# Optimization experiments

Hardware: AMD Instinct MI355X
Metric: run time of the kernel (lower is better)

## Reference

```python
import jax, jax.numpy as jnp
import numpy as np

L = 4          # layers_num
N_HIPER = 30   # n_hiper
S = 4096       # number of ray samples
D = 768        # embedding width (hardcoded in source)


def setup_inputs() -> dict:
    key = jax.random.key(0)
    k1, k2, k3 = jax.random.split(key, 3)
    # coords must lie in [-L, L] so grid indices stay in [0, 2L]
    samples = jax.random.uniform(k1, (S, 2), minval=-float(L), maxval=float(L), dtype=jnp.float32)
    last_point = jax.random.uniform(k2, (2,), minval=-float(L), maxval=float(L), dtype=jnp.float32)
    embeddings = jax.random.normal(k3, (2 * L + 1, 2 * L + 1, N_HIPER + 1, D), dtype=jnp.float32)
    return {"samples": samples, "last_point": last_point, "embeddings": embeddings}


def reference(samples, last_point, embeddings):
    x, y = samples[:, 0], samples[:, 1]
    # fractional parts computed BEFORE the +L shift, exactly as in the source
    dx = (x - jnp.floor(x))[:, None, None]  # [S,1,1]
    dy = (y - jnp.floor(y))[:, None, None]
    xs, ys = x + L, y + L
    fx = jnp.floor(xs).astype(jnp.int32)
    cx = jnp.ceil(xs).astype(jnp.int32)
    fy = jnp.floor(ys).astype(jnp.int32)
    cy = jnp.ceil(ys).astype(jnp.int32)
    # batched bilinear gather: each corner lookup is [S, N_HIPER+1, D]
    above = embeddings[fx, cy] * (1.0 - dx) + embeddings[cx, cy] * dx
    below = embeddings[fx, fy] * (1.0 - dx) + embeddings[cx, fy] * dx
    emb = below * (1.0 - dy) + above * dy  # [S, N_HIPER+1, D]

    # distance to next sample; last sample measures to last_point
    nxt = jnp.concatenate([samples[1:], last_point[None, :]], axis=0)
    dists = jnp.linalg.norm(nxt - samples, axis=1)  # [S]

    density = jax.nn.relu(emb[:, N_HIPER])          # [S, D] (per-channel density)
    dd = density * dists[:, None]                   # [S, D]
    # Ti uses EXCLUSIVE cumsum: summed_density is updated after Ti is read
    cum_excl = jnp.concatenate(
        [jnp.zeros((1, D), dd.dtype), jnp.cumsum(dd, axis=0)[:-1]], axis=0
    )
    weights = jnp.exp(-cum_excl) * (1.0 - jnp.exp(-dd))  # Ti * alpha, [S, D]
    # sum_s weights[s,d] * emb[s,n,d]  -> [N_HIPER, D]
    return jnp.einsum("sd,snd->nd", weights, emb[:, :N_HIPER])
```

## Files before the change

kernel.cpp:

```cpp
#include <hip/hip_runtime.h>
#include <math.h>

#define NS 4096
#define DD 768
#define NH 30
#define NCH 31
#define NCELL 81
#define NBLK 256
#define NTHR 384
#define CS 16
#define NPART 6
#define SPP 683
#define NW (NCELL*DD)
#define NACC (NCELL*NPART)

__global__ __launch_bounds__(NTHR) void pass1_kernel(
    const float* __restrict__ samples, const float* __restrict__ last_point,
    const float* __restrict__ emb,
    int4* __restrict__ cells, float4* __restrict__ coefs,
    float* __restrict__ ddbuf, float* __restrict__ chunk_sum,
    float* __restrict__ W)
{
    __shared__ int4   s_cells[CS];
    __shared__ float4 s_coefs[CS];
    __shared__ float  s_dist[CS];

    const int t  = threadIdx.x;
    const int b  = blockIdx.x;
    const int d0 = 2*t;

    if (t < CS) {
        const int s = b*CS + t;
        float x = samples[2*s+0], y = samples[2*s+1];
        float xs = x + 4.0f, ys = y + 4.0f;
        int fx = (int)floorf(xs), cx = (int)ceilf(xs);
        int fy = (int)floorf(ys), cy = (int)ceilf(ys);
        float dx = x - floorf(x), dy = y - floorf(y);
        float nx, ny;
        if (s == NS-1) { nx = last_point[0]; ny = last_point[1]; }
        else           { nx = samples[2*s+2]; ny = samples[2*s+3]; }
        float ex = nx - x, ey = ny - y;
        s_dist[t] = sqrtf(ex*ex + ey*ey);
        int4 cl = make_int4(fx*9+fy, cx*9+fy, fx*9+cy, cx*9+cy);
        float4 cf = make_float4((1.f-dx)*(1.f-dy), dx*(1.f-dy),
                                (1.f-dx)*dy,       dx*dy);
        s_cells[t] = cl; s_coefs[t] = cf;
        cells[s] = cl;   coefs[s]  = cf;
    }
    { int g = b*NTHR + t; if (g < NW) W[g] = 0.f; }
    __syncthreads();

    float sx = 0.f, sy = 0.f;
    #pragma unroll
    for (int i = 0; i < CS; ++i) {
        int4 cl = s_cells[i]; float4 cf = s_coefs[i]; float dist = s_dist[i];
        const int off = NH*DD + d0;
        float2 e0 = *(const float2*)(emb + cl.x*NCH*DD + off);
        float2 e1 = *(const float2*)(emb + cl.y*NCH*DD + off);
        float2 e2 = *(const float2*)(emb + cl.z*NCH*DD + off);
        float2 e3 = *(const float2*)(emb + cl.w*NCH*DD + off);
        float vx = e0.x*cf.x + e1.x*cf.y + e2.x*cf.z + e3.x*cf.w;
        float vy = e0.y*cf.x + e1.y*cf.y + e2.y*cf.z + e3.y*cf.w;
        float ddx = fmaxf(vx, 0.f) * dist;
        float ddy = fmaxf(vy, 0.f) * dist;
        *(float2*)(ddbuf + (b*CS + i)*DD + d0) = make_float2(ddx, ddy);
        sx += ddx; sy += ddy;
    }
    *(float2*)(chunk_sum + b*DD + d0) = make_float2(sx, sy);
}

__global__ __launch_bounds__(64) void scan_kernel(
    const float* __restrict__ chunk_sum, float* __restrict__ offs) {
    const int d    = blockIdx.x;
    const int lane = threadIdx.x;
    float v[4];
    #pragma unroll
    for (int k = 0; k < 4; ++k)
        v[k] = chunk_sum[(lane*4 + k)*DD + d];
    float tot = (v[0] + v[1]) + (v[2] + v[3]);
    float x = tot;
    #pragma unroll
    for (int off = 1; off < 64; off <<= 1) {
        float y = __shfl_up(x, off);
        if (lane >= off) x += y;
    }
    float run = x - tot;
    #pragma unroll
    for (int k = 0; k < 4; ++k) {
        offs[(lane*4 + k)*DD + d] = run;
        run += v[k];
    }
}

__global__ __launch_bounds__(NTHR) void w_kernel(
    const float* __restrict__ ddbuf, const float* __restrict__ offs,
    float* __restrict__ w) {
    const int t  = threadIdx.x;
    const int b  = blockIdx.x;
    const int d0 = 2*t;
    float2 cum = *(const float2*)(offs + b*DD + d0);
    float Ex = __expf(-cum.x), Ey = __expf(-cum.y);
    #pragma unroll
    for (int i = 0; i < CS; ++i) {
        float2 dd = *(const float2*)(ddbuf + (b*CS + i)*DD + d0);
        float fx = __expf(-dd.x), fy = __expf(-dd.y);
        *(float2*)(w + (b*CS + i)*DD + d0) =
            make_float2(Ex * (1.f - fx), Ey * (1.f - fy));
        Ex *= fx; Ey *= fy;
    }
}

__global__ __launch_bounds__(256) void wacc_kernel(
    const int4* __restrict__ cells, const float4* __restrict__ coefs,
    const float* __restrict__ w, float* __restrict__ W) {
    __shared__ int   s_idx[SPP];
    __shared__ float s_cf[SPP];
    __shared__ int   s_cnt;
    const int g    = blockIdx.x / NPART;
    const int part = blockIdx.x % NPART;
    const int t    = threadIdx.x;
    if (t == 0) s_cnt = 0;
    __syncthreads();
    const int s_beg = part * SPP;
    const int s_end = min(NS, s_beg + SPP);
    for (int s = s_beg + t; s < s_end; s += 256) {
        int4 cl = cells[s]; float4 cf = coefs[s];
        float c = 0.f;
        if (cl.x == g) c += cf.x;
        if (cl.y == g) c += cf.y;
        if (cl.z == g) c += cf.z;
        if (cl.w == g) c += cf.w;
        if (c != 0.f) {
            int idx = atomicAdd(&s_cnt, 1);
            s_idx[idx] = s;
            s_cf[idx]  = c;
        }
    }
    __syncthreads();
    const int cnt = s_cnt;
    float a0 = 0.f, a1 = 0.f, a2 = 0.f;
    for (int j = 0; j < cnt; ++j) {
        const float* wr = w + (long)s_idx[j]*DD;
        const float  c  = s_cf[j];
        a0 += c * wr[t];
        a1 += c * wr[t + 256];
        a2 += c * wr[t + 512];
    }
    atomicAdd(&W[g*DD + t      ], a0);
    atomicAdd(&W[g*DD + t + 256], a1);
    atomicAdd(&W[g*DD + t + 512], a2);
}

__global__ __launch_bounds__(256) void final_kernel(
    const float* __restrict__ emb, const float* __restrict__ W,
    float* __restrict__ out) {
    const int n    = blockIdx.x / 3;
    const int part = blockIdx.x % 3;
    const int d    = part*256 + threadIdx.x;
    float a0 = 0.f, a1 = 0.f, a2 = 0.f, a3 = 0.f;
    int g = 0;
    #pragma unroll 4
    for (; g + 4 <= 80; g += 4) {
        a0 += W[(g+0)*DD + d] * emb[((g+0)*NCH + n)*DD + d];
        a1 += W[(g+1)*DD + d] * emb[((g+1)*NCH + n)*DD + d];
        a2 += W[(g+2)*DD + d] * emb[((g+2)*NCH + n)*DD + d];
        a3 += W[(g+3)*DD + d] * emb[((g+3)*NCH + n)*DD + d];
    }
    a0 += W[80*DD + d] * emb[(80*NCH + n)*DD + d];
    out[n*DD + d] = (a0 + a1) + (a2 + a3);
}

extern "C" void kernel_launch(void* const* d_in, const int* in_sizes, int n_in,
                              void* d_out, int out_size, void* d_ws, size_t ws_size,
                              hipStream_t stream) {
    const float* samples    = (const float*)d_in[0];
    const float* last_point = (const float*)d_in[1];
    const float* emb        = (const float*)d_in[2];
    float* out = (float*)d_out;

    char* ws = (char*)d_ws;
    int4*   cells  = (int4*)ws;     ws += (size_t)NS*sizeof(int4);
    float4* coefs  = (float4*)ws;   ws += (size_t)NS*sizeof(float4);
    float*  chunk_sum = (float*)ws; ws += (size_t)NBLK*DD*sizeof(float);
    float*  offs   = (float*)ws;    ws += (size_t)NBLK*DD*sizeof(float);
    float*  Wbuf   = (float*)ws;    ws += (size_t)NW*sizeof(float);
    float*  ddbuf  = (float*)ws;    ws += (size_t)NS*DD*sizeof(float);
    float*  wmat   = (float*)ws;    ws += (size_t)NS*DD*sizeof(float);

    pass1_kernel<<<NBLK, NTHR, 0, stream>>>(samples, last_point, emb,
                                            cells, coefs, ddbuf, chunk_sum,
                                            Wbuf);
    scan_kernel<<<DD, 64, 0, stream>>>(chunk_sum, offs);
    w_kernel<<<NBLK, NTHR, 0, stream>>>(ddbuf, offs, wmat);
    wacc_kernel<<<NACC, 256, 0, stream>>>(cells, coefs, wmat, Wbuf);
    final_kernel<<<NH*3, 256, 0, stream>>>(emb, Wbuf, out);
}
```

Before: 38.08 us.

## Replace additive density scan with multiplicative transmittance scan and drop w kernel

pass1 now computes per-chunk local transmittance products and unscaled weights directly. The scan runs over products of exp factors instead of sums. The chunk scale is applied inside the accumulation kernel, which removes the separate w_kernel and one full S×D intermediate buffer. Loads are widened to float4 and the final kernel is reorganised to one block per output row. The cost is a product-based scan that can underflow differently from the sum-then-exp form, plus a changed chunk and thread geometry.

Result: slower. 49.57 us (+30.2%).

```diff
diff --git a/kernel.cpp b/kernel.cpp
--- a/kernel.cpp
+++ b/kernel.cpp
@@ -6,9 +6,9 @@
 #define NH 30
 #define NCH 31
 #define NCELL 81
-#define NBLK 256
-#define NTHR 384
-#define CS 16
+#define NBLK 512
+#define NTHR 192
+#define CS 8
 #define NPART 6
 #define SPP 683
 #define NW (NCELL*DD)
@@ -18,7 +18,7 @@
     const float* __restrict__ samples, const float* __restrict__ last_point,
     const float* __restrict__ emb,
     int4* __restrict__ cells, float4* __restrict__ coefs,
-    float* __restrict__ ddbuf, float* __restrict__ chunk_sum,
+    float* __restrict__ u, float* __restrict__ Ebuf,
     float* __restrict__ W)
 {
     __shared__ int4   s_cells[CS];
@@ -27,7 +27,7 @@
 
     const int t  = threadIdx.x;
     const int b  = blockIdx.x;
-    const int d0 = 2*t;
+    const int d0 = 4*t;
 
     if (t < CS) {
         const int s = b*CS + t;
@@ -47,83 +47,78 @@
         s_cells[t] = cl; s_coefs[t] = cf;
         cells[s] = cl;   coefs[s]  = cf;
     }
-    { int g = b*NTHR + t; if (g < NW) W[g] = 0.f; }
+    {
+        int g = b*NTHR + t; if (g < NW) W[g] = 0.f;
+    }
     __syncthreads();
 
-    float sx = 0.f, sy = 0.f;
+    float4 E = make_float4(1.f, 1.f, 1.f, 1.f);
     #pragma unroll
     for (int i = 0; i < CS; ++i) {
         int4 cl = s_cells[i]; float4 cf = s_coefs[i]; float dist = s_dist[i];
         const int off = NH*DD + d0;
-        float2 e0 = *(const float2*)(emb + cl.x*NCH*DD + off);
-        float2 e1 = *(const float2*)(emb + cl.y*NCH*DD + off);
-        float2 e2 = *(const float2*)(emb + cl.z*NCH*DD + off);
-        float2 e3 = *(const float2*)(emb + cl.w*NCH*DD + off);
+        float4 e0 = *(const float4*)(emb + cl.x*NCH*DD + off);
+        float4 e1 = *(const float4*)(emb + cl.y*NCH*DD + off);
+        float4 e2 = *(const float4*)(emb + cl.z*NCH*DD + off);
+        float4 e3 = *(const float4*)(emb + cl.w*NCH*DD + off);
         float vx = e0.x*cf.x + e1.x*cf.y + e2.x*cf.z + e3.x*cf.w;
         float vy = e0.y*cf.x + e1.y*cf.y + e2.y*cf.z + e3.y*cf.w;
-        float ddx = fmaxf(vx, 0.f) * dist;
-        float ddy = fmaxf(vy, 0.f) * dist;
-        *(float2*)(ddbuf + (b*CS + i)*DD + d0) = make_float2(ddx, ddy);
-        sx += ddx; sy += ddy;
+        float vz = e0.z*cf.x + e1.z*cf.y + e2.z*cf.z + e3.z*cf.w;
+        float vw = e0.w*cf.x + e1.w*cf.y + e2.w*cf.z + e3.w*cf.w;
+        float fx_ = __expf(-fmaxf(vx, 0.f) * dist);
+        float fy_ = __expf(-fmaxf(vy, 0.f) * dist);
+        float fz_ = __expf(-fmaxf(vz, 0.f) * dist);
+        float fw_ = __expf(-fmaxf(vw, 0.f) * dist);
+        *(float4*)(u + (b*CS + i)*DD + d0) =
+            make_float4(E.x*(1.f-fx_), E.y*(1.f-fy_),
+                        E.z*(1.f-fz_), E.w*(1.f-fw_));
+        E.x *= fx_; E.y *= fy_; E.z *= fz_; E.w *= fw_;
     }
-    *(float2*)(chunk_sum + b*DD + d0) = make_float2(sx, sy);
+    *(float4*)(Ebuf + b*DD + d0) = E;
 }
 
 __global__ __launch_bounds__(64) void scan_kernel(
-    const float* __restrict__ chunk_sum, float* __restrict__ offs) {
+    const float* __restrict__ Ebuf, float* __restrict__ scale) {
     const int d    = blockIdx.x;
     const int lane = threadIdx.x;
-    float v[4];
+    float v[8];
+    float tot = 1.f;
     #pragma unroll
-    for (int k = 0; k < 4; ++k)
-        v[k] = chunk_sum[(lane*4 + k)*DD + d];
-    float tot = (v[0] + v[1]) + (v[2] + v[3]);
+    for (int k = 0; k < 8; ++k) {
+        v[k] = Ebuf[(lane*8 + k)*DD + d];
+        tot *= v[k];
+    }
     float x = tot;
     #pragma unroll
     for (int off = 1; off < 64; off <<= 1) {
         float y = __shfl_up(x, off);
-        if (lane >= off) x += y;
+        if (lane >= off) x *= y;
     }
-    float run = x - tot;
+    float run = __shfl_up(x, 1);
+    if (lane == 0) run = 1.f;
     #pragma unroll
-    for (int k = 0; k < 4; ++k) {
-        offs[(lane*4 + k)*DD + d] = run;
-        run += v[k];
+    for (int k = 0; k < 8; ++k) {
+        scale[(lane*8 + k)*DD + d] = run;
+        run *= v[k];
     }
 }
 
-__global__ __launch_bounds__(NTHR) void w_kernel(
-    const float* __restrict__ ddbuf, const float* __restrict__ offs,
-    float* __restrict__ w) {
-    const int t  = threadIdx.x;
-    const int b  = blockIdx.x;
-    const int d0 = 2*t;
-    float2 cum = *(const float2*)(offs + b*DD + d0);
-    float Ex = __expf(-cum.x), Ey = __expf(-cum.y);
-    #pragma unroll
-    for (int i = 0; i < CS; ++i) {
-        float2 dd = *(const float2*)(ddbuf + (b*CS + i)*DD + d0);
-        float fx = __expf(-dd.x), fy = __expf(-dd.y);
-        *(float2*)(w + (b*CS + i)*DD + d0) =
-            make_float2(Ex * (1.f - fx), Ey * (1.f - fy));
-        Ex *= fx; Ey *= fy;
-    }
-}
-
-__global__ __launch_bounds__(256) void wacc_kernel(
+__global__ __launch_bounds__(NTHR) void wacc_kernel(
     const int4* __restrict__ cells, const float4* __restrict__ coefs,
-    const float* __restrict__ w, float* __restrict__ W) {
+    const float* __restrict__ u, const float* __restrict__ scale,
+    float* __restrict__ W) {
     __shared__ int   s_idx[SPP];
     __shared__ float s_cf[SPP];
     __shared__ int   s_cnt;
     const int g    = blockIdx.x / NPART;
     const int part = blockIdx.x % NPART;
     const int t    = threadIdx.x;
+    const int d0   = 4*t;
     if (t == 0) s_cnt = 0;
     __syncthreads();
     const int s_beg = part * SPP;
     const int s_end = min(NS, s_beg + SPP);
-    for (int s = s_beg + t; s < s_end; s += 256) {
+    for (int s = s_beg + t; s < s_end; s += NTHR) {
         int4 cl = cells[s]; float4 cf = coefs[s];
         float c = 0.f;
         if (cl.x == g) c += cf.x;
@@ -138,36 +133,40 @@
     }
     __syncthreads();
     const int cnt = s_cnt;
-    float a0 = 0.f, a1 = 0.f, a2 = 0.f;
+    float4 a = make_float4(0.f, 0.f, 0.f, 0.f);
     for (int j = 0; j < cnt; ++j) {
-        const float* wr = w + (long)s_idx[j]*DD;
-        const float  c  = s_cf[j];
-        a0 += c * wr[t];
-        a1 += c * wr[t + 256];
-        a2 += c * wr[t + 512];
+        const int   s = s_idx[j];
+        const float c = s_cf[j];
+        const int   ch = s >> 3;
+        float4 uv = *(const float4*)(u + (long)s*DD + d0);
+        float4 sc = *(const float4*)(scale + (long)ch*DD + d0);
+        a.x += c * sc.x * uv.x;
+        a.y += c * sc.y * uv.y;
+        a.z += c * sc.z * uv.z;
+        a.w += c * sc.w * uv.w;
     }
-    atomicAdd(&W[g*DD + t      ], a0);
-    atomicAdd(&W[g*DD + t + 256], a1);
-    atomicAdd(&W[g*DD + t + 512], a2);
+    atomicAdd(&W[g*DD + d0 + 0], a.x);
+    atomicAdd(&W[g*DD + d0 + 1], a.y);
+    atomicAdd(&W[g*DD + d0 + 2], a.z);
+    atomicAdd(&W[g*DD + d0 + 3], a.w);
 }
 
-__global__ __launch_bounds__(256) void final_kernel(
+__global__ __launch_bounds__(NTHR) void final_kernel(
     const float* __restrict__ emb, const float* __restrict__ W,
     float* __restrict__ out) {
-    const int n    = blockIdx.x / 3;
-    const int part = blockIdx.x % 3;
-    const int d    = part*256 + threadIdx.x;
-    float a0 = 0.f, a1 = 0.f, a2 = 0.f, a3 = 0.f;
-    int g = 0;
-    #pragma unroll 4
-    for (; g + 4 <= 80; g += 4) {
-        a0 += W[(g+0)*DD + d] * emb[((g+0)*NCH + n)*DD + d];
-        a1 += W[(g+1)*DD + d] * emb[((g+1)*NCH + n)*DD + d];
-        a2 += W[(g+2)*DD + d] * emb[((g+2)*NCH + n)*DD + d];
-        a3 += W[(g+3)*DD + d] * emb[((g+3)*NCH + n)*DD + d];
+    const int n  = blockIdx.x;
+    const int d0 = 4*threadIdx.x;
+    float4 a = make_float4(0.f, 0.f, 0.f, 0.f);
+    #pragma unroll 3
+    for (int g = 0; g < NCELL; ++g) {
+        float4 Wv = *(const float4*)(W + g*DD + d0);
+        float4 Tv = *(const float4*)(emb + (g*NCH + n)*DD + d0);
+        a.x += Wv.x*Tv.x;
+        a.y += Wv.y*Tv.y;
+        a.z += Wv.z*Tv.z;
+        a.w += Wv.w*Tv.w;
     }
-    a0 += W[80*DD + d] * emb[(80*NCH + n)*DD + d];
-    out[n*DD + d] = (a0 + a1) + (a2 + a3);
+    *(float4*)(out + n*DD + d0) = a;
 }
 
 extern "C" void kernel_launch(void* const* d_in, const int* in_sizes, int n_in,
@@ -179,19 +178,16 @@
     float* out = (float*)d_out;
 
     char* ws = (char*)d_ws;
-    int4*   cells  = (int4*)ws;     ws += (size_t)NS*sizeof(int4);
-    float4* coefs  = (float4*)ws;   ws += (size_t)NS*sizeof(float4);
-    float*  chunk_sum = (float*)ws; ws += (size_t)NBLK*DD*sizeof(float);
-    float*  offs   = (float*)ws;    ws += (size_t)NBLK*DD*sizeof(float);
-    float*  Wbuf   = (float*)ws;    ws += (size_t)NW*sizeof(float);
-    float*  ddbuf  = (float*)ws;    ws += (size_t)NS*DD*sizeof(float);
-    float*  wmat   = (float*)ws;    ws += (size_t)NS*DD*sizeof(float);
+    int4*   cells = (int4*)ws;     ws += (size_t)NS*sizeof(int4);
+    float4* coefs = (float4*)ws;   ws += (size_t)NS*sizeof(float4);
+    float*  Ebuf  = (float*)ws;    ws += (size_t)NBLK*DD*sizeof(float);
+    float*  scale = (float*)ws;    ws += (size_t)NBLK*DD*sizeof(float);
+    float*  Wbuf  = (float*)ws;    ws += (size_t)NW*sizeof(float);
+    float*  umat  = (float*)ws;    ws += (size_t)NS*DD*sizeof(float);
 
     pass1_kernel<<<NBLK, NTHR, 0, stream>>>(samples, last_point, emb,
-                                            cells, coefs, ddbuf, chunk_sum,
-                                            Wbuf);
-    scan_kernel<<<DD, 64, 0, stream>>>(chunk_sum, offs);
-    w_kernel<<<NBLK, NTHR, 0, stream>>>(ddbuf, offs, wmat);
-    wacc_kernel<<<NACC, 256, 0, stream>>>(cells, coefs, wmat, Wbuf);
-    final_kernel<<<NH*3, 256, 0, stream>>>(emb, Wbuf, out);
+                                            cells, coefs, umat, Ebuf, Wbuf);
+    scan_kernel<<<DD, 64, 0, stream>>>(Ebuf, scale);
+    wacc_kernel<<<NACC, NTHR, 0, stream>>>(cells, coefs, umat, scale, Wbuf);
+    final_kernel<<<NH, NTHR, 0, stream>>>(emb, Wbuf, out);
 }
```

## Fold transmittance into pass1 and scan chunk products, drop w_kernel

Applied to the files above, without the earlier changes.

Pass1 now computes the per-chunk local weights directly, as chunk-local transmittance times alpha, and stores each chunk's transmittance product. The scan switches from an additive prefix over density sums to a multiplicative prefix over those products. The accumulation kernel applies the per-chunk scale while reading the local weights. This removes one kernel launch plus a full 4096x768 write and re-read of the intermediate buffer. In exchange it adds a scale load per sample row in wacc, and multiplying many exponentials may underflow differently than the exp of a sum.

After: 40.94 us. 7.5% more time.

```diff
diff --git a/kernel.cpp b/kernel.cpp
--- a/kernel.cpp
+++ b/kernel.cpp
@@ -18,7 +18,7 @@
     const float* __restrict__ samples, const float* __restrict__ last_point,
     const float* __restrict__ emb,
     int4* __restrict__ cells, float4* __restrict__ coefs,
-    float* __restrict__ ddbuf, float* __restrict__ chunk_sum,
+    float* __restrict__ u, float* __restrict__ Ebuf,
     float* __restrict__ W)
 {
     __shared__ int4   s_cells[CS];
@@ -50,7 +50,7 @@
     { int g = b*NTHR + t; if (g < NW) W[g] = 0.f; }
     __syncthreads();
 
-    float sx = 0.f, sy = 0.f;
+    float Ex = 1.f, Ey = 1.f;
     #pragma unroll
     for (int i = 0; i < CS; ++i) {
         int4 cl = s_cells[i]; float4 cf = s_coefs[i]; float dist = s_dist[i];
@@ -61,58 +61,45 @@
         float2 e3 = *(const float2*)(emb + cl.w*NCH*DD + off);
         float vx = e0.x*cf.x + e1.x*cf.y + e2.x*cf.z + e3.x*cf.w;
         float vy = e0.y*cf.x + e1.y*cf.y + e2.y*cf.z + e3.y*cf.w;
-        float ddx = fmaxf(vx, 0.f) * dist;
-        float ddy = fmaxf(vy, 0.f) * dist;
-        *(float2*)(ddbuf + (b*CS + i)*DD + d0) = make_float2(ddx, ddy);
-        sx += ddx; sy += ddy;
+        float fx_ = __expf(-fmaxf(vx, 0.f) * dist);
+        float fy_ = __expf(-fmaxf(vy, 0.f) * dist);
+        *(float2*)(u + (b*CS + i)*DD + d0) =
+            make_float2(Ex*(1.f - fx_), Ey*(1.f - fy_));
+        Ex *= fx_; Ey *= fy_;
     }
-    *(float2*)(chunk_sum + b*DD + d0) = make_float2(sx, sy);
+    *(float2*)(Ebuf + b*DD + d0) = make_float2(Ex, Ey);
 }
 
 __global__ __launch_bounds__(64) void scan_kernel(
-    const float* __restrict__ chunk_sum, float* __restrict__ offs) {
+    const float* __restrict__ Ebuf, float* __restrict__ scale) {
     const int d    = blockIdx.x;
     const int lane = threadIdx.x;
     float v[4];
+    float tot = 1.f;
     #pragma unroll
-    for (int k = 0; k < 4; ++k)
-        v[k] = chunk_sum[(lane*4 + k)*DD + d];
-    float tot = (v[0] + v[1]) + (v[2] + v[3]);
+    for (int k = 0; k < 4; ++k) {
+        v[k] = Ebuf[(lane*4 + k)*DD + d];
+        tot *= v[k];
+    }
     float x = tot;
     #pragma unroll
     for (int off = 1; off < 64; off <<= 1) {
         float y = __shfl_up(x, off);
-        if (lane >= off) x += y;
+        if (lane >= off) x *= y;
     }
-    float run = x - tot;
+    float run = __shfl_up(x, 1);
+    if (lane == 0) run = 1.f;
     #pragma unroll
     for (int k = 0; k < 4; ++k) {
-        offs[(lane*4 + k)*DD + d] = run;
-        run += v[k];
-    }
-}
-
-__global__ __launch_bounds__(NTHR) void w_kernel(
-    const float* __restrict__ ddbuf, const float* __restrict__ offs,
-    float* __restrict__ w) {
-    const int t  = threadIdx.x;
-    const int b  = blockIdx.x;
-    const int d0 = 2*t;
-    float2 cum = *(const float2*)(offs + b*DD + d0);
-    float Ex = __expf(-cum.x), Ey = __expf(-cum.y);
-    #pragma unroll
-    for (int i = 0; i < CS; ++i) {
-        float2 dd = *(const float2*)(ddbuf + (b*CS + i)*DD + d0);
-        float fx = __expf(-dd.x), fy = __expf(-dd.y);
-        *(float2*)(w + (b*CS + i)*DD + d0) =
-            make_float2(Ex * (1.f - fx), Ey * (1.f - fy));
-        Ex *= fx; Ey *= fy;
+        scale[(lane*4 + k)*DD + d] = run;
+        run *= v[k];
     }
 }
 
 __global__ __launch_bounds__(256) void wacc_kernel(
     const int4* __restrict__ cells, const float4* __restrict__ coefs,
-    const float* __restrict__ w, float* __restrict__ W) {
+    const float* __restrict__ u, const float* __restrict__ scale,
+    float* __restrict__ W) {
     __shared__ int   s_idx[SPP];
     __shared__ float s_cf[SPP];
     __shared__ int   s_cnt;
@@ -140,11 +127,14 @@
     const int cnt = s_cnt;
     float a0 = 0.f, a1 = 0.f, a2 = 0.f;
     for (int j = 0; j < cnt; ++j) {
-        const float* wr = w + (long)s_idx[j]*DD;
-        const float  c  = s_cf[j];
-        a0 += c * wr[t];
-        a1 += c * wr[t + 256];
-        a2 += c * wr[t + 512];
+        const int   s  = s_idx[j];
+        const float c  = s_cf[j];
+        const int   ch = s >> 4;
+        const float* ur = u     + (long)s*DD;
+        const float* sr = scale + (long)ch*DD;
+        a0 += c * sr[t      ] * ur[t      ];
+        a1 += c * sr[t + 256] * ur[t + 256];
+        a2 += c * sr[t + 512] * ur[t + 512];
     }
     atomicAdd(&W[g*DD + t      ], a0);
     atomicAdd(&W[g*DD + t + 256], a1);
@@ -179,19 +169,16 @@
     float* out = (float*)d_out;
 
     char* ws = (char*)d_ws;
-    int4*   cells  = (int4*)ws;     ws += (size_t)NS*sizeof(int4);
-    float4* coefs  = (float4*)ws;   ws += (size_t)NS*sizeof(float4);
-    float*  chunk_sum = (float*)ws; ws += (size_t)NBLK*DD*sizeof(float);
-    float*  offs   = (float*)ws;    ws += (size_t)NBLK*DD*sizeof(float);
-    float*  Wbuf   = (float*)ws;    ws += (size_t)NW*sizeof(float);
-    float*  ddbuf  = (float*)ws;    ws += (size_t)NS*DD*sizeof(float);
-    float*  wmat   = (float*)ws;    ws += (size_t)NS*DD*sizeof(float);
+    int4*   cells = (int4*)ws;     ws += (size_t)NS*sizeof(int4);
+    float4* coefs = (float4*)ws;   ws += (size_t)NS*sizeof(float4);
+    float*  Ebuf  = (float*)ws;    ws += (size_t)NBLK*DD*sizeof(float);
+    float*  scale = (float*)ws;    ws += (size_t)NBLK*DD*sizeof(float);
+    float*  Wbuf  = (float*)ws;    ws += (size_t)NW*sizeof(float);
+    float*  umat  = (float*)ws;    ws += (size_t)NS*DD*sizeof(float);
 
     pass1_kernel<<<NBLK, NTHR, 0, stream>>>(samples, last_point, emb,
-                                            cells, coefs, ddbuf, chunk_sum,
-                                            Wbuf);
-    scan_kernel<<<DD, 64, 0, stream>>>(chunk_sum, offs);
-    w_kernel<<<NBLK, NTHR, 0, stream>>>(ddbuf, offs, wmat);
-    wacc_kernel<<<NACC, 256, 0, stream>>>(cells, coefs, wmat, Wbuf);
+                                            cells, coefs, umat, Ebuf, Wbuf);
+    scan_kernel<<<DD, 64, 0, stream>>>(Ebuf, scale);
+    wacc_kernel<<<NACC, 256, 0, stream>>>(cells, coefs, umat, scale, Wbuf);
     final_kernel<<<NH*3, 256, 0, stream>>>(emb, Wbuf, out);
 }
```
